# Performance work log

Measured on AMD Instinct MI355X. Metric: run time of the kernel, lower is better.

Reference implementation:

```python
import jax, jax.numpy as jnp
import numpy as np

B, N, C, K, D, H = 4, 16000, 128, 16, 4, 512
EPS = 1e-5


def _bn(x, g, b, m, v):
    # eval-mode BatchNorm1d over channel dim (applied to flattened B*N rows)
    return (x - m) * jax.lax.rsqrt(v + EPS) * g + b


def _ffn(x, W1, b1, W2, g, b, m, v):
    h = jax.nn.gelu(jnp.einsum('bnc,ch->bnh', x, W1) + b1)
    y = jnp.einsum('bnh,hc->bnc', h, W2)  # second linear has no bias
    return _bn(y, g, b, m, v)


def _vector_feature(x, knn):
    # knn edge max-pooling: max_k ( x[b, knn[b,n,k], :] - x[b, n, :] )
    gathered = jnp.take_along_axis(x[:, :, None, :], knn[:, :, :, None], axis=1)  # (B,N,K,C)
    return jnp.max(gathered - x[:, :, None, :], axis=2)


def _vfr(x, knn, W, g, b, m, v):
    y = jnp.einsum('bnc,cd->bnd', x, W)
    y = _vector_feature(y, knn)
    return _bn(y, g, b, m, v)


def setup_inputs():
    key = jax.random.key(0)
    ks = jax.random.split(key, 16)
    s = 0.05
    return {
        'x': jax.random.normal(ks[0], (B, N, C), jnp.float32),
        'pe': jax.random.normal(ks[1], (B, N, C), jnp.float32),
        'knn': jax.random.randint(ks[2], (B, N, K), 0, N, dtype=jnp.int32),
        # mlp (the single leading FFN)
        'mlp_W1': jax.random.normal(ks[3], (C, H), jnp.float32) * s,
        'mlp_b1': jnp.zeros((H,), jnp.float32),
        'mlp_W2': jax.random.normal(ks[4], (H, C), jnp.float32) * s,
        'mlp_g': jax.random.uniform(ks[5], (C,), jnp.float32, 0.5, 1.5),
        'mlp_beta': jnp.zeros((C,), jnp.float32),
        'mlp_m': jnp.zeros((C,), jnp.float32),
        'mlp_v': jnp.ones((C,), jnp.float32),
        # per-depth VFR params (stacked over depth D)
        'vfr_W': jax.random.normal(ks[6], (D, C, C), jnp.float32) * s,
        'vfr_g': jax.random.uniform(ks[7], (D, C), jnp.float32, 0.5, 1.5),
        'vfr_beta': jnp.zeros((D, C), jnp.float32),
        'vfr_m': jnp.zeros((D, C), jnp.float32),
        'vfr_v': jnp.ones((D, C), jnp.float32),
        # per-depth FFN params
        'ffn_W1': jax.random.normal(ks[8], (D, C, H), jnp.float32) * s,
        'ffn_b1': jnp.zeros((D, H), jnp.float32),
        'ffn_W2': jax.random.normal(ks[9], (D, H, C), jnp.float32) * s,
        'ffn_g': jax.random.uniform(ks[10], (D, C), jnp.float32, 0.5, 1.5),
        'ffn_beta': jnp.zeros((D, C), jnp.float32),
        'ffn_m': jnp.zeros((D, C), jnp.float32),
        'ffn_v': jnp.ones((D, C), jnp.float32),
    }


def reference(x, pe, knn,
              mlp_W1, mlp_b1, mlp_W2, mlp_g, mlp_beta, mlp_m, mlp_v,
              vfr_W, vfr_g, vfr_beta, vfr_m, vfr_v,
              ffn_W1, ffn_b1, ffn_W2, ffn_g, ffn_beta, ffn_m, ffn_v):
    # drop_path is identity in eval mode
    x = x + _ffn(x, mlp_W1, mlp_b1, mlp_W2, mlp_g, mlp_beta, mlp_m, mlp_v)
    for i in range(D):
        x = x + pe
        x = x + _vfr(x, knn, vfr_W[i], vfr_g[i], vfr_beta[i], vfr_m[i], vfr_v[i])
        x = x + _ffn(x, ffn_W1[i], ffn_b1[i], ffn_W2[i], ffn_g[i], ffn_beta[i], ffn_m[i], ffn_v[i])
    return x
```

## Files before the change

kernel.cpp:

```cpp
#include <hip/hip_runtime.h>
#include <hip/hip_bf16.h>

typedef __attribute__((ext_vector_type(8))) short bf16x8;
typedef __attribute__((ext_vector_type(4))) short bf16x4;
typedef __attribute__((ext_vector_type(4))) float f32x4;

#define B_ 4
#define N_ 16000
#define C_ 128
#define K_ 16
#define D_ 4
#define H_ 512
#define R_ (B_*N_)
#define EPSV 1e-5f

__device__ __forceinline__ ushort f2bf(float f) {
    uint32_t b = __builtin_bit_cast(uint32_t, f);
    b += 0x7fffu + ((b >> 16) & 1u);
    return (ushort)(b >> 16);
}
__device__ __forceinline__ float bf2f(ushort u) {
    return __builtin_bit_cast(float, (uint32_t)u << 16);
}
__device__ __forceinline__ uint pk2bf(float lo, float hi) {
    return (uint)f2bf(lo) | ((uint)f2bf(hi) << 16);
}
__device__ __forceinline__ float gelu_fast(float v) {
    float v2 = v * v;
    float u = v * fmaf(0.0356774081f, v2, 0.7978845608f);
    float e = __expf(-2.0f * u);
    return v * __builtin_amdgcn_rcpf(1.0f + e);
}
__device__ __forceinline__ void gll16(const void* g, void* l) {
    __builtin_amdgcn_global_load_lds(
        (__attribute__((address_space(1))) void*)g,
        (__attribute__((address_space(3))) void*)l, 16, 0, 0);
}

__global__ void prep_kernel(
    const float* __restrict__ mlp_W1, const float* __restrict__ mlp_b1,
    const float* __restrict__ mlp_W2, const float* __restrict__ mlp_g,
    const float* __restrict__ mlp_be, const float* __restrict__ mlp_m,
    const float* __restrict__ mlp_v,
    const float* __restrict__ vfr_W, const float* __restrict__ vfr_g,
    const float* __restrict__ vfr_be, const float* __restrict__ vfr_m,
    const float* __restrict__ vfr_v,
    const float* __restrict__ ffn_W1, const float* __restrict__ ffn_b1,
    const float* __restrict__ ffn_W2, const float* __restrict__ ffn_g,
    const float* __restrict__ ffn_be, const float* __restrict__ ffn_m,
    const float* __restrict__ ffn_v,
    ushort* __restrict__ w1t, ushort* __restrict__ w2p, ushort* __restrict__ wvs,
    float* __restrict__ b1a, float* __restrict__ fs, float* __restrict__ fb,
    float* __restrict__ vs, float* __restrict__ vb)
{
    int i = blockIdx.x * 256 + threadIdx.x;
    const int NW = 5 * H_ * C_;
    if (i < NW) {
        int f = i / (H_*C_), e = i % (H_*C_);
        int h = e / C_, c = e % C_;
        const float* src = (f == 0) ? mlp_W1 : ffn_W1 + (size_t)(f-1)*C_*H_;
        w1t[i] = f2bf(src[(size_t)c*H_ + h]);
        return;
    }
    i -= NW;
    if (i < NW) {
        int f = i / (H_*C_), e = i % (H_*C_);
        int c = e / H_, p = e % H_;
        int s = p & 31, lam = s >> 3, j = s & 7;
        int h = (p & ~31) + lam*4 + (j & 3) + ((j >> 2) << 4);
        const float* src = (f == 0) ? mlp_W2 : ffn_W2 + (size_t)(f-1)*H_*C_;
        w2p[i] = f2bf(src[(size_t)h*C_ + c]);
        return;
    }
    i -= NW;
    if (i < D_*C_*C_) {
        int d = i / (C_*C_), e = i % (C_*C_);
        int co = e / C_, p = e % C_;
        int s = p & 31, lam = s >> 3, j = s & 7;
        int k = (p & ~31) + lam*4 + (j & 3) + ((j >> 2) << 4);
        wvs[i] = f2bf(vfr_W[(size_t)d*C_*C_ + (size_t)k*C_ + co]);
        return;
    }
    i -= D_*C_*C_;
    if (i < 5*H_) {
        int f = i / H_, h = i % H_;
        b1a[i] = (f == 0) ? mlp_b1[h] : ffn_b1[(f-1)*H_ + h];
        return;
    }
    i -= 5*H_;
    if (i < 5*C_) {
        int f = i / C_, c = i % C_;
        float g  = (f==0) ? mlp_g[c]  : ffn_g[(f-1)*C_ + c];
        float be = (f==0) ? mlp_be[c] : ffn_be[(f-1)*C_ + c];
        float m  = (f==0) ? mlp_m[c]  : ffn_m[(f-1)*C_ + c];
        float v  = (f==0) ? mlp_v[c]  : ffn_v[(f-1)*C_ + c];
        float s = g * rsqrtf(v + EPSV);
        fs[i] = s; fb[i] = be - m * s;
        return;
    }
    i -= 5*C_;
    if (i < D_*C_) {
        float s = vfr_g[i] * rsqrtf(vfr_v[i] + EPSV);
        vs[i] = s; vb[i] = vfr_be[i] - vfr_m[i] * s;
    }
}

template<bool ADD_PE, bool NEXT_T>
__global__ __launch_bounds__(256, 2) void ffn_kernel(
    const float* __restrict__ xin, float* __restrict__ xout,
    const float* __restrict__ pe,
    const ushort* __restrict__ W1t,
    const ushort* __restrict__ W2p,
    const float* __restrict__ b1,
    const float* __restrict__ bns, const float* __restrict__ bnb,
    const ushort* __restrict__ Wvs,
    ushort* __restrict__ tout)
{
    __shared__ __attribute__((aligned(16))) char lds[65536];

    const int tid  = threadIdx.x;
    const int m0   = blockIdx.x * 128;
    const int wv   = tid >> 6;
    const int lane = tid & 63;
    const int lr   = lane & 15;
    const int lh   = lane >> 4;

    auto stageW = [&](int hc, int buf) {
        char* base = lds + buf * 32768;
        const int h0 = hc * 64;
        #pragma unroll
        for (int i = 0; i < 4; ++i) {
            int row = i*16 + wv*4 + (lane >> 4);
            const char* src = (const char*)(W1t + (size_t)(h0 + row) * C_)
                            + (((lane & 15) * 16) ^ ((row & 7) << 4));
            gll16(src, base + i*4096 + wv*1024);
        }
        #pragma unroll
        for (int i = 0; i < 4; ++i) {
            int row = i*32 + wv*8 + (lane >> 3);
            const char* src = (const char*)(W2p + (size_t)row * H_ + h0)
                            + (((lane & 7) * 16) ^ ((row & 7) << 4));
            gll16(src, base + 16384 + i*4096 + wv*1024);
        }
    };

    stageW(0, 0);

    bf16x8 xa[2][4];
    #pragma unroll
    for (int mt = 0; mt < 2; ++mt) {
        const float* xrow = xin + (size_t)(m0 + wv*32 + mt*16 + lr) * C_ + lh*8;
        #pragma unroll
        for (int kk = 0; kk < 4; ++kk) {
            float4 v0 = *(const float4*)(xrow + kk*32);
            float4 v1 = *(const float4*)(xrow + kk*32 + 4);
            uint p0 = pk2bf(v0.x, v0.y), p1 = pk2bf(v0.z, v0.w);
            uint p2 = pk2bf(v1.x, v1.y), p3 = pk2bf(v1.z, v1.w);
            uint4 u = {p0, p1, p2, p3};
            xa[mt][kk] = __builtin_bit_cast(bf16x8, u);
        }
    }

    f32x4 acc2[2][8];
    #pragma unroll
    for (int mt = 0; mt < 2; ++mt)
        #pragma unroll
        for (int i = 0; i < 8; ++i) acc2[mt][i] = (f32x4){0.f,0.f,0.f,0.f};

    __syncthreads();

    for (int hc = 0; hc < 8; ++hc) {
        const int h0  = hc * 64;
        const int buf = hc & 1;
        if (hc < 7) stageW(hc + 1, buf ^ 1);

        char* W1s = lds + buf * 32768;
        char* W2s = W1s + 16384;

        f32x4 acc1[2][4];
        #pragma unroll
        for (int mt = 0; mt < 2; ++mt)
            #pragma unroll
            for (int i = 0; i < 4; ++i) acc1[mt][i] = (f32x4){0.f,0.f,0.f,0.f};
        #pragma unroll
        for (int kk = 0; kk < 4; ++kk) {
            int kb = kk*64 + lh*16;
            #pragma unroll
            for (int nf = 0; nf < 4; ++nf) {
                int rb = nf*16 + lr;
                bf16x8 w1 = *(bf16x8*)(W1s + rb*256 + (kb ^ ((rb&7)<<4)));
                #pragma unroll
                for (int mt = 0; mt < 2; ++mt)
                    acc1[mt][nf] = __builtin_amdgcn_mfma_f32_16x16x32_bf16(
                        w1, xa[mt][kk], acc1[mt][nf], 0, 0, 0);
            }
        }
        bf16x4 pa[2][4];
        #pragma unroll
        for (int nf = 0; nf < 4; ++nf) {
            float4 bias = *(const float4*)(b1 + h0 + nf*16 + lh*4);
            #pragma unroll
            for (int mt = 0; mt < 2; ++mt) {
                uint q0 = pk2bf(gelu_fast(acc1[mt][nf][0] + bias.x),
                                gelu_fast(acc1[mt][nf][1] + bias.y));
                uint q1 = pk2bf(gelu_fast(acc1[mt][nf][2] + bias.z),
                                gelu_fast(acc1[mt][nf][3] + bias.w));
                uint2 u = {q0, q1};
                pa[mt][nf] = __builtin_bit_cast(bf16x4, u);
            }
        }
        #pragma unroll
        for (int g = 0; g < 2; ++g) {
            bf16x8 af[2];
            #pragma unroll
            for (int mt = 0; mt < 2; ++mt)
                af[mt] = __builtin_shufflevector(pa[mt][2*g], pa[mt][2*g+1],
                                                 0,1,2,3,4,5,6,7);
            int kb = g*64 + lh*16;
            #pragma unroll
            for (int nf = 0; nf < 8; ++nf) {
                int rb = nf*16 + lr;
                bf16x8 w2 = *(bf16x8*)(W2s + rb*128 + (kb ^ ((rb&7)<<4)));
                #pragma unroll
                for (int mt = 0; mt < 2; ++mt)
                    acc2[mt][nf] = __builtin_amdgcn_mfma_f32_16x16x32_bf16(
                        w2, af[mt], acc2[mt][nf], 0, 0, 0);
            }
        }
        __syncthreads();
    }

    if (NEXT_T) {
        #pragma unroll
        for (int i = 0; i < 8; ++i) {
            int r = i*16 + wv*4 + (lane >> 4);
            const char* src = (const char*)(Wvs + (size_t)r * C_)
                            + (((lane & 15) * 16) ^ ((r & 7) << 4));
            gll16(src, lds + i*4096 + wv*1024);
        }
    }

    bf16x4 pa2[2][8];
    #pragma unroll
    for (int mt = 0; mt < 2; ++mt) {
        const int row = m0 + wv*32 + mt*16 + lr;
        #pragma unroll
        for (int nf = 0; nf < 8; ++nf) {
            int c0 = nf*16 + lh*4;
            float4 sv = *(const float4*)(bns + c0);
            float4 bv = *(const float4*)(bnb + c0);
            float4 xi = *(const float4*)(xin + (size_t)row * C_ + c0);
            if (ADD_PE) {
                float4 pv = *(const float4*)(pe + (size_t)row * C_ + c0);
                xi.x += pv.x; xi.y += pv.y; xi.z += pv.z; xi.w += pv.w;
            }
            float4 xo;
            xo.x = xi.x + acc2[mt][nf][0] * sv.x + bv.x;
            xo.y = xi.y + acc2[mt][nf][1] * sv.y + bv.y;
            xo.z = xi.z + acc2[mt][nf][2] * sv.z + bv.z;
            xo.w = xi.w + acc2[mt][nf][3] * sv.w + bv.w;
            *(float4*)(xout + (size_t)row * C_ + c0) = xo;
            if (NEXT_T) {
                uint2 u = {pk2bf(xo.x, xo.y), pk2bf(xo.z, xo.w)};
                pa2[mt][nf] = __builtin_bit_cast(bf16x4, u);
            }
        }
    }

    if (NEXT_T) {
        __syncthreads();
        f32x4 acc3[2][8];
        #pragma unroll
        for (int mt = 0; mt < 2; ++mt)
            #pragma unroll
            for (int i = 0; i < 8; ++i) acc3[mt][i] = (f32x4){0.f,0.f,0.f,0.f};
        #pragma unroll
        for (int g = 0; g < 4; ++g) {
            bf16x8 af[2];
            #pragma unroll
            for (int mt = 0; mt < 2; ++mt)
                af[mt] = __builtin_shufflevector(pa2[mt][2*g], pa2[mt][2*g+1],
                                                 0,1,2,3,4,5,6,7);
            int kb = g*64 + lh*16;
            #pragma unroll
            for (int nf = 0; nf < 8; ++nf) {
                int rb = nf*16 + lr;
                bf16x8 wvf = *(bf16x8*)(lds + rb*256 + (kb ^ ((rb&7)<<4)));
                #pragma unroll
                for (int mt = 0; mt < 2; ++mt)
                    acc3[mt][nf] = __builtin_amdgcn_mfma_f32_16x16x32_bf16(
                        af[mt], wvf, acc3[mt][nf], 0, 0, 0);
            }
        }
        #pragma unroll
        for (int mt = 0; mt < 2; ++mt) {
            #pragma unroll
            for (int nf = 0; nf < 8; ++nf) {
                int col = nf*16 + lr;
                #pragma unroll
                for (int j = 0; j < 4; ++j) {
                    int trow = m0 + wv*32 + mt*16 + lh*4 + j;
                    tout[(size_t)trow * C_ + col] = f2bf(acc3[mt][nf][j]);
                }
            }
        }
    }
}

__global__ __launch_bounds__(256) void vfr_gather_kernel(
    float* __restrict__ x, const ushort* __restrict__ t,
    const int* __restrict__ knn,
    const float* __restrict__ s, const float* __restrict__ bb)
{
    const int wv   = threadIdx.x >> 6;
    const int lane = threadIdx.x & 63;
    const int p = blockIdx.x * 4 + wv;
    const int b = p / N_;
    const int base = b * N_;
    const int* kp = knn + (size_t)p * K_;
    const uint* trow = (const uint*)t;

    uint cen = trow[(size_t)p * 64 + lane];
    float c0 = bf2f((ushort)(cen & 0xffffu));
    float c1 = bf2f((ushort)(cen >> 16));
    float m0v = -INFINITY, m1v = -INFINITY;
    #pragma unroll
    for (int k = 0; k < K_; ++k) {
        int idx = kp[k];
        uint g = trow[(size_t)(base + idx) * 64 + lane];
        m0v = fmaxf(m0v, bf2f((ushort)(g & 0xffffu)));
        m1v = fmaxf(m1v, bf2f((ushort)(g >> 16)));
    }
    m0v -= c0; m1v -= c1;

    int c = lane * 2;
    float2 sv = *(const float2*)(s + c);
    float2 bv = *(const float2*)(bb + c);
    size_t o = (size_t)p * C_ + c;
    float2 xv = *(const float2*)(x + o);
    xv.x += m0v * sv.x + bv.x;
    xv.y += m1v * sv.y + bv.y;
    *(float2*)(x + o) = xv;
}

extern "C" void kernel_launch(void* const* d_in, const int* in_sizes, int n_in,
                              void* d_out, int out_size, void* d_ws, size_t ws_size,
                              hipStream_t stream) {
    const float* x      = (const float*)d_in[0];
    const float* pe     = (const float*)d_in[1];
    const int*   knn    = (const int*)d_in[2];
    const float* mlp_W1 = (const float*)d_in[3];
    const float* mlp_b1 = (const float*)d_in[4];
    const float* mlp_W2 = (const float*)d_in[5];
    const float* mlp_g  = (const float*)d_in[6];
    const float* mlp_be = (const float*)d_in[7];
    const float* mlp_m  = (const float*)d_in[8];
    const float* mlp_v  = (const float*)d_in[9];
    const float* vfr_W  = (const float*)d_in[10];
    const float* vfr_g  = (const float*)d_in[11];
    const float* vfr_be = (const float*)d_in[12];
    const float* vfr_m  = (const float*)d_in[13];
    const float* vfr_v  = (const float*)d_in[14];
    const float* ffn_W1 = (const float*)d_in[15];
    const float* ffn_b1 = (const float*)d_in[16];
    const float* ffn_W2 = (const float*)d_in[17];
    const float* ffn_g  = (const float*)d_in[18];
    const float* ffn_be = (const float*)d_in[19];
    const float* ffn_m  = (const float*)d_in[20];
    const float* ffn_v  = (const float*)d_in[21];
    float* out = (float*)d_out;

    char* ws = (char*)d_ws;
    ushort* tbuf = (ushort*)ws;  ws += (size_t)R_ * C_ * 2;
    ushort* w1t  = (ushort*)ws;  ws += (size_t)5 * H_ * C_ * 2;
    ushort* w2p  = (ushort*)ws;  ws += (size_t)5 * C_ * H_ * 2;
    ushort* wvs  = (ushort*)ws;  ws += (size_t)D_ * C_ * C_ * 2;
    float*  b1a  = (float*)ws;   ws += (size_t)5 * H_ * 4;
    float*  fs   = (float*)ws;   ws += (size_t)5 * C_ * 4;
    float*  fb   = (float*)ws;   ws += (size_t)5 * C_ * 4;
    float*  vs   = (float*)ws;   ws += (size_t)D_ * C_ * 4;
    float*  vb   = (float*)ws;   ws += (size_t)D_ * C_ * 4;

    const int prep_items = 2*(5*H_*C_) + D_*C_*C_ + 5*H_ + 5*C_ + D_*C_;
    prep_kernel<<<(prep_items + 255) / 256, 256, 0, stream>>>(
        mlp_W1, mlp_b1, mlp_W2, mlp_g, mlp_be, mlp_m, mlp_v,
        vfr_W, vfr_g, vfr_be, vfr_m, vfr_v,
        ffn_W1, ffn_b1, ffn_W2, ffn_g, ffn_be, ffn_m, ffn_v,
        w1t, w2p, wvs, b1a, fs, fb, vs, vb);

    ffn_kernel<true, true><<<R_/128, 256, 0, stream>>>(
        x, out, pe, w1t, w2p, b1a, fs, fb, wvs, tbuf);

    for (int d = 0; d < D_; ++d) {
        vfr_gather_kernel<<<R_/4, 256, 0, stream>>>(
            out, tbuf, knn, vs + d * C_, vb + d * C_);
        if (d < D_ - 1) {
            ffn_kernel<true, true><<<R_/128, 256, 0, stream>>>(
                out, out, pe,
                w1t + (size_t)(d+1) * H_ * C_, w2p + (size_t)(d+1) * C_ * H_,
                b1a + (d+1) * H_, fs + (d+1) * C_, fb + (d+1) * C_,
                wvs + (size_t)(d+1) * C_ * C_, tbuf);
        } else {
            ffn_kernel<false, false><<<R_/128, 256, 0, stream>>>(
                out, out, pe,
                w1t + (size_t)(d+1) * H_ * C_, w2p + (size_t)(d+1) * C_ * H_,
                b1a + (d+1) * H_, fs + (d+1) * C_, fb + (d+1) * C_,
                wvs, tbuf);
        }
    }
}
```

Baseline: 355.4 us.

## Prefetch next VFR weight during last FFN chunk with fine-grained vmcnt waits

```diff
diff --git a/kernel.cpp b/kernel.cpp
--- a/kernel.cpp
+++ b/kernel.cpp
@@ -143,6 +143,16 @@
             gll16(src, base + 16384 + i*4096 + wv*1024);
         }
     };
+    auto stageWv = [&](int buf) {
+        char* base = lds + buf * 32768;
+        #pragma unroll
+        for (int i = 0; i < 8; ++i) {
+            int r = i*16 + wv*4 + (lane >> 4);
+            const char* src = (const char*)(Wvs + (size_t)r * C_)
+                            + (((lane & 15) * 16) ^ ((r & 7) << 4));
+            gll16(src, base + i*4096 + wv*1024);
+        }
+    };
 
     stageW(0, 0);
 
@@ -167,12 +177,28 @@
         #pragma unroll
         for (int i = 0; i < 8; ++i) acc2[mt][i] = (f32x4){0.f,0.f,0.f,0.f};
 
-    __syncthreads();
-
+    #pragma unroll 1
     for (int hc = 0; hc < 8; ++hc) {
         const int h0  = hc * 64;
         const int buf = hc & 1;
-        if (hc < 7) stageW(hc + 1, buf ^ 1);
+
+        float4 biasv[4];
+        #pragma unroll
+        for (int nf = 0; nf < 4; ++nf)
+            biasv[nf] = *(const float4*)(b1 + h0 + nf*16 + lh*4);
+        __builtin_amdgcn_sched_barrier(0);
+
+        if (hc < 7) {
+            stageW(hc + 1, buf ^ 1);
+            asm volatile("s_waitcnt vmcnt(12)" ::: "memory");
+        } else if (NEXT_T) {
+            stageWv(buf ^ 1);
+            asm volatile("s_waitcnt vmcnt(12)" ::: "memory");
+        } else {
+            asm volatile("s_waitcnt vmcnt(4)" ::: "memory");
+        }
+        __builtin_amdgcn_s_barrier();
+        __builtin_amdgcn_sched_barrier(0);
 
         char* W1s = lds + buf * 32768;
         char* W2s = W1s + 16384;
@@ -198,13 +224,12 @@
         bf16x4 pa[2][4];
         #pragma unroll
         for (int nf = 0; nf < 4; ++nf) {
-            float4 bias = *(const float4*)(b1 + h0 + nf*16 + lh*4);
             #pragma unroll
             for (int mt = 0; mt < 2; ++mt) {
-                uint q0 = pk2bf(gelu_fast(acc1[mt][nf][0] + bias.x),
-                                gelu_fast(acc1[mt][nf][1] + bias.y));
-                uint q1 = pk2bf(gelu_fast(acc1[mt][nf][2] + bias.z),
-                                gelu_fast(acc1[mt][nf][3] + bias.w));
+                uint q0 = pk2bf(gelu_fast(acc1[mt][nf][0] + biasv[nf].x),
+                                gelu_fast(acc1[mt][nf][1] + biasv[nf].y));
+                uint q1 = pk2bf(gelu_fast(acc1[mt][nf][2] + biasv[nf].z),
+                                gelu_fast(acc1[mt][nf][3] + biasv[nf].w));
                 uint2 u = {q0, q1};
                 pa[mt][nf] = __builtin_bit_cast(bf16x4, u);
             }
@@ -227,17 +252,16 @@
                         w2, af[mt], acc2[mt][nf], 0, 0, 0);
             }
         }
-        __syncthreads();
+
+        __builtin_amdgcn_sched_barrier(0);
+        asm volatile("s_waitcnt lgkmcnt(0)" ::: "memory");
+        __builtin_amdgcn_s_barrier();
     }
 
     if (NEXT_T) {
-        #pragma unroll
-        for (int i = 0; i < 8; ++i) {
-            int r = i*16 + wv*4 + (lane >> 4);
-            const char* src = (const char*)(Wvs + (size_t)r * C_)
-                            + (((lane & 15) * 16) ^ ((r & 7) << 4));
-            gll16(src, lds + i*4096 + wv*1024);
-        }
+        asm volatile("s_waitcnt vmcnt(0)" ::: "memory");
+        __builtin_amdgcn_s_barrier();
+        __builtin_amdgcn_sched_barrier(0);
     }
 
     bf16x4 pa2[2][8];
@@ -268,7 +292,6 @@
     }
 
     if (NEXT_T) {
-        __syncthreads();
         f32x4 acc3[2][8];
         #pragma unroll
         for (int mt = 0; mt < 2; ++mt)
```

Result: no change. 356.4 us (+0.3%).
